# Kernel optimization log

Measured on AMD Instinct MI355X. Metric: run time of the kernel, lower is better.

Reference implementation:

```python
import jax, jax.numpy as jnp
import numpy as np

D_MODEL = 512
D_INNER = 1024  # expand * d_model
D_STATE = 128
D_CONV = 4
DT_RANK = 32
DT_MIN, DT_MAX, DT_FLOOR = 0.001, 0.1, 1e-4


def setup_inputs() -> dict:
    key = jax.random.key(0)
    ks = jax.random.split(key, 8)
    B, S = 2, 1024
    return {
        "x": jax.random.normal(ks[0], (B, S, D_MODEL), jnp.float32),
        "W_in": jax.random.normal(ks[1], (D_MODEL, 2 * D_INNER), jnp.float32) * 0.02,
        "conv_w": jax.random.normal(ks[2], (D_INNER, 1, D_CONV), jnp.float32) * 0.1,
        "conv_b": jnp.zeros((D_INNER,), jnp.float32),
        "W_x": jax.random.normal(ks[3], (D_INNER, DT_RANK + 2 * D_STATE), jnp.float32) * 0.02,
        "W_dt": jax.random.normal(ks[4], (DT_RANK, D_INNER), jnp.float32) * 0.02,
        "b_dt": jnp.zeros((D_INNER,), jnp.float32),
        "W_out": jax.random.normal(ks[5], (D_INNER, D_MODEL), jnp.float32) * 0.02,
    }


def _mamba_forward(x, W_in, conv_w, conv_b, W_x, W_dt, b_dt, W_out):
    Bsz, S, _ = x.shape
    xr = x @ W_in                              # [B,S,2*d_inner]
    xs, res = jnp.split(xr, 2, axis=-1)        # each [B,S,d_inner]

    # depthwise causal conv (torch pads both sides by d_conv-1 then truncates
    # to seq_len, which equals a left-pad-only causal conv)
    xc = xs.transpose(0, 2, 1)                 # [B,d_inner,S]
    xc = jax.lax.conv_general_dilated(
        xc, conv_w, window_strides=(1,), padding=[(D_CONV - 1, 0)],
        feature_group_count=D_INNER)
    u = (xc + conv_b[None, :, None]).transpose(0, 2, 1)  # [B,S,d_inner]

    dbl = u @ W_x                              # [B,S,dt_rank+2*d_state]
    dt, Bm, Cm = jnp.split(dbl, [DT_RANK, DT_RANK + D_STATE], axis=-1)
    dt = dt @ W_dt + b_dt                      # [B,S,d_inner]
    dt = jnp.clip(jax.nn.softplus(dt + DT_FLOOR), DT_MIN, DT_MAX)

    # selective scan: h_t = h_{t-1}*(1-dt_t) + x_t (outer) B_t ; y_t = h_t . C_t
    def step(h, inp):
        x_t, dt_t, B_t, C_t = inp              # [B,d_inner],[B,d_inner],[B,N],[B,N]
        h = h * (1.0 - dt_t)[..., None] + x_t[..., None] * B_t[:, None, :]
        y = jnp.einsum('bdn,bn->bd', h, C_t)
        return h, y

    h0 = jnp.zeros((Bsz, D_INNER, D_STATE), u.dtype)
    xs_t = (u.transpose(1, 0, 2), dt.transpose(1, 0, 2),
            Bm.transpose(1, 0, 2), Cm.transpose(1, 0, 2))
    _, ys = jax.lax.scan(step, h0, xs_t)       # ys: [S,B,d_inner]

    y = ys.transpose(1, 0, 2) + res
    return y @ W_out                           # [B,S,d_model]


def reference(x, W_in, conv_w, conv_b, W_x, W_dt, b_dt, W_out):
    return _mamba_forward(x, W_in, conv_w, conv_b, W_x, W_dt, b_dt, W_out)
```

## Files before the change

### kernel.cpp

```cpp
#include <hip/hip_runtime.h>
#include <math.h>

#define S_LEN 1024
#define BATCH 2
#define DM 512
#define DI 1024
#define DS 128
#define DTR 32
#define CL 64
#define NC (S_LEN / CL)

typedef unsigned short ushortT;
typedef __attribute__((ext_vector_type(8))) short short8;
typedef __attribute__((ext_vector_type(4))) float f32x4;

__device__ __forceinline__ ushortT f2b(float f) {
  unsigned u = __builtin_bit_cast(unsigned, f);
  unsigned r = (u + 0x7fff + ((u >> 16) & 1)) >> 16;
  return (ushortT)r;
}
__device__ __forceinline__ float b2f(ushortT h) {
  return __builtin_bit_cast(float, (unsigned)h << 16);
}

#define GLOAD16(g, l)                                                     \
  __builtin_amdgcn_global_load_lds(                                       \
      (const __attribute__((address_space(1))) void*)(g),                 \
      (__attribute__((address_space(3))) void*)(l), 16, 0, 0)

template<int MODE>
__global__ __launch_bounds__(256) void gemm64(
    const ushortT* __restrict__ A, const ushortT* __restrict__ Bt,
    void* __restrict__ Cout, int N, int K, int ldc, int nbx) {
  __shared__ ushortT As[2][64 * 32];
  __shared__ ushortT Bs[2][64 * 32];
  const int nwg = gridDim.x;
  const int bid = blockIdx.x;
  const int flat = (bid & 7) * (nwg >> 3) + (bid >> 3);
  const int bxi = flat % nbx, byi = flat / nbx;
  const int bm = byi * 64, bn = bxi * 64;
  const int tid = threadIdx.x;
  const int l = tid & 63, w = tid >> 6;
  const int wr = w >> 1, wc = w & 1;
  const int srow = tid >> 2, scol = (tid & 3) * 8;
  const ushortT* gA = A + (size_t)(bm + srow) * K + scol;
  const ushortT* gB = Bt + (size_t)(bn + srow) * K + scol;
  f32x4 acc[2][2] = {};
  const int nt = K >> 5;
  GLOAD16(gA, &As[0][(size_t)tid * 8]);
  GLOAD16(gB, &Bs[0][(size_t)tid * 8]);
  __syncthreads();
  int cur = 0;
  for (int t = 0; t < nt; ++t) {
    if (t + 1 < nt) {
      GLOAD16(gA + (t + 1) * 32, &As[cur ^ 1][(size_t)tid * 8]);
      GLOAD16(gB + (t + 1) * 32, &Bs[cur ^ 1][(size_t)tid * 8]);
    }
    short8 a[2], b[2];
#pragma unroll
    for (int m = 0; m < 2; ++m)
      a[m] = *(const short8*)&As[cur][(wr * 32 + m * 16 + (l & 15)) * 32 + (l >> 4) * 8];
#pragma unroll
    for (int n = 0; n < 2; ++n)
      b[n] = *(const short8*)&Bs[cur][(wc * 32 + n * 16 + (l & 15)) * 32 + (l >> 4) * 8];
#pragma unroll
    for (int m = 0; m < 2; ++m)
#pragma unroll
      for (int n = 0; n < 2; ++n)
        acc[m][n] = __builtin_amdgcn_mfma_f32_16x16x32_bf16(a[m], b[n], acc[m][n], 0, 0, 0);
    __syncthreads();
    cur ^= 1;
  }
#pragma unroll
  for (int m = 0; m < 2; ++m) {
    int grow = bm + wr * 32 + m * 16 + (l >> 4) * 4;
#pragma unroll
    for (int n = 0; n < 2; ++n) {
      int gcol = bn + wc * 32 + n * 16 + (l & 15);
      if (gcol >= N) continue;
#pragma unroll
      for (int i = 0; i < 4; ++i) {
        float v = acc[m][n][i];
        if (MODE == 1)
          ((ushortT*)Cout)[(size_t)(grow + i) * ldc + gcol] = f2b(v);
        else
          ((float*)Cout)[(size_t)(grow + i) * ldc + gcol] = v;
      }
    }
  }
}

__global__ __launch_bounds__(256) void prep_all(
    const float* __restrict__ W_in, const float* __restrict__ W_x,
    const float* __restrict__ W_out, const float* __restrict__ x,
    ushortT* __restrict__ Wt_in, ushortT* __restrict__ Wt_x,
    ushortT* __restrict__ Wt_out, ushortT* __restrict__ x_bf) {
  __shared__ float tb[32][33];
  int bid = blockIdx.x;
  int tx = threadIdx.x, ty = threadIdx.y;
  const float* in; ushortT* out; int K, N, bx, by;
  if (bid < 1024)      { in = W_in;  out = Wt_in;  K = 512;  N = 2048; bx = bid & 63; by = bid >> 6; }
  else if (bid < 1408) { int t2 = bid - 1024; in = W_x;   out = Wt_x;   K = 1024; N = 288;  bx = t2 % 12; by = t2 / 12; }
  else if (bid < 1920) { int t2 = bid - 1408; in = W_out; out = Wt_out; K = 1024; N = 512;  bx = t2 % 16; by = t2 / 16; }
  else {
    int i = (bid - 1920) * 256 + ty * 32 + tx;
    float4 v = ((const float4*)x)[i];
    ushort4 o; o.x = f2b(v.x); o.y = f2b(v.y); o.z = f2b(v.z); o.w = f2b(v.w);
    ((ushort4*)x_bf)[i] = o;
    return;
  }
  int n0 = bx * 32, k0 = by * 32;
  int flat = ty * 32 + tx;
  if (n0 < N) {
#pragma unroll
    for (int i = 0; i < 4; ++i)
      tb[ty + 8 * i][tx] = in[(size_t)(k0 + ty + 8 * i) * N + n0 + tx];
    __syncthreads();
#pragma unroll
    for (int j = 0; j < 2; ++j) {
      int idx = j * 256 + flat;
      int r = idx >> 4, c2 = idx & 15;
      ushort2 o;
      o.x = f2b(tb[2 * c2][r]);
      o.y = f2b(tb[2 * c2 + 1][r]);
      *(ushort2*)&out[(size_t)(n0 + r) * K + k0 + 2 * c2] = o;
    }
  } else {
    ushort2 z; z.x = 0; z.y = 0;
#pragma unroll
    for (int j = 0; j < 2; ++j) {
      int idx = j * 256 + flat;
      int r = idx >> 4, c2 = idx & 15;
      *(ushort2*)&out[(size_t)(n0 + r) * K + k0 + 2 * c2] = z;
    }
  }
}

__global__ __launch_bounds__(256) void conv_kernel(
    const ushortT* __restrict__ xr, const float* __restrict__ w,
    const float* __restrict__ b, ushortT* __restrict__ u) {
  int idx = blockIdx.x * blockDim.x + threadIdx.x;
  int g = idx & 255;
  int s = (idx >> 8) & (S_LEN - 1);
  int bb = idx >> 18;
  int d = g * 4;
  float4 bias = *(const float4*)&b[d];
  float4 w0 = *(const float4*)&w[(d + 0) * 4];
  float4 w1 = *(const float4*)&w[(d + 1) * 4];
  float4 w2 = *(const float4*)&w[(d + 2) * 4];
  float4 w3 = *(const float4*)&w[(d + 3) * 4];
  float a0 = bias.x, a1 = bias.y, a2 = bias.z, a3 = bias.w;
  const ushortT* xs = xr + (size_t)(bb * S_LEN) * (2 * DI) + d;
#pragma unroll
  for (int k = 0; k < 4; ++k) {
    int si = s - 3 + k;
    if (si >= 0) {
      ushort4 v = *(const ushort4*)&xs[(size_t)si * (2 * DI)];
      float wk0 = ((const float*)&w0)[k], wk1 = ((const float*)&w1)[k];
      float wk2 = ((const float*)&w2)[k], wk3 = ((const float*)&w3)[k];
      a0 = fmaf(b2f(v.x), wk0, a0);
      a1 = fmaf(b2f(v.y), wk1, a1);
      a2 = fmaf(b2f(v.z), wk2, a2);
      a3 = fmaf(b2f(v.w), wk3, a3);
    }
  }
  ushort4 o; o.x = f2b(a0); o.y = f2b(a1); o.z = f2b(a2); o.w = f2b(a3);
  *(ushort4*)&u[(size_t)idx * 4] = o;
}

__global__ __launch_bounds__(256) void megachunk(
    const float* __restrict__ dbl, const float* __restrict__ W_dt,
    const float* __restrict__ b_dt, const ushortT* __restrict__ u_bf,
    float* __restrict__ D, ushortT* __restrict__ ut,
    ushortT* __restrict__ zb) {
  __shared__ ushortT Btl[128][72];
  __shared__ float   Dl[64][66];
  __shared__ ushortT utl[64][72];
  __shared__ float   dtl[64][36];
  __shared__ ushortT Wl[32][68];
  const int t = threadIdx.x;
  const int dg = blockIdx.x, bc = blockIdx.y;
  const int b = bc >> 4, c = bc & 15;
  const size_t rowbase = (size_t)(b * S_LEN + c * CL) * DI + dg * 64;

#pragma unroll
  for (int j = 0; j < 8; ++j) {
    int idx4 = j * 256 + t;
    int s = idx4 >> 5, n4 = (idx4 & 31) * 4;
    float4 v = *(const float4*)&dbl[(size_t)(bc * 64 + s) * 288 + 32 + n4];
    Btl[n4][s] = f2b(v.x); Btl[n4 + 1][s] = f2b(v.y);
    Btl[n4 + 2][s] = f2b(v.z); Btl[n4 + 3][s] = f2b(v.w);
  }
#pragma unroll
  for (int j = 0; j < 2; ++j) {
    int idx4 = j * 256 + t;
    int s = idx4 >> 3, k4 = (idx4 & 7) * 4;
    *(float4*)&dtl[s][k4] = *(const float4*)&dbl[(size_t)(bc * 64 + s) * 288 + k4];
  }
#pragma unroll
  for (int j = 0; j < 4; ++j) {
    int idx2 = j * 256 + t;
    int k = idx2 >> 5, d2 = (idx2 & 31) * 2;
    float2 v = *(const float2*)&W_dt[(size_t)k * DI + dg * 64 + d2];
    Wl[k][d2] = f2b(v.x); Wl[k][d2 + 1] = f2b(v.y);
  }
  __syncthreads();

  {
    int d = t & 63, sq = t >> 6;
    float wreg[32];
#pragma unroll
    for (int k = 0; k < 32; ++k) wreg[k] = b2f(Wl[k][d]);
    float bias = b_dt[dg * 64 + d] + 1e-4f;
#pragma unroll 4
    for (int j = 0; j < 16; ++j) {
      int s = sq * 16 + j;
      float acc = bias;
#pragma unroll
      for (int k = 0; k < 32; ++k) acc = fmaf(dtl[s][k], wreg[k], acc);
      acc = (acc > 20.f) ? acc : log1pf(expf(acc));
      acc = fminf(fmaxf(acc, 0.001f), 0.1f);
      Dl[d][s] = 1.f - acc;
    }
  }
  __syncthreads();

  if (t < 64) {
    float cum = 1.f;
#pragma unroll 16
    for (int s = 0; s < CL; ++s) { cum *= Dl[t][s]; Dl[t][s] = cum; }
  }
  __syncthreads();

#pragma unroll
  for (int j = 0; j < 2; ++j) {
    int idx8 = j * 256 + t;
    int s = idx8 >> 3, d8 = (idx8 & 7) * 8;
    float4 raw = *(const float4*)&u_bf[rowbase + (size_t)s * DI + d8];
    const ushortT* up = (const ushortT*)&raw;
#pragma unroll
    for (int k = 0; k < 8; ++k)
      utl[d8 + k][s] = f2b(b2f(up[k]) / Dl[d8 + k][s]);
  }
  __syncthreads();

  {
    const int l = t & 63, w = t >> 6;
    f32x4 acc[8] = {};
#pragma unroll
    for (int kk = 0; kk < 2; ++kk) {
      short8 a = *(const short8*)&utl[w * 16 + (l & 15)][kk * 32 + (l >> 4) * 8];
#pragma unroll
      for (int n = 0; n < 8; ++n) {
        short8 bb = *(const short8*)&Btl[n * 16 + (l & 15)][kk * 32 + (l >> 4) * 8];
        acc[n] = __builtin_amdgcn_mfma_f32_16x16x32_bf16(a, bb, acc[n], 0, 0, 0);
      }
    }
#pragma unroll
    for (int n = 0; n < 8; ++n) {
      int gn = n * 16 + (l & 15);
#pragma unroll
      for (int i = 0; i < 4; ++i) {
        int d = dg * 64 + w * 16 + (l >> 4) * 4 + i;
        zb[(((size_t)(b * DI + d)) * NC + c) * 128 + gn] = f2b(acc[n][i]);
      }
    }
  }

#pragma unroll
  for (int j = 0; j < 4; ++j) {
    int idx4 = j * 256 + t;
    int s = idx4 >> 4, d4 = (idx4 & 15) * 4;
    float4 v;
    v.x = Dl[d4][s]; v.y = Dl[d4 + 1][s]; v.z = Dl[d4 + 2][s]; v.w = Dl[d4 + 3][s];
    *(float4*)&D[rowbase + (size_t)s * DI + d4] = v;
  }
#pragma unroll
  for (int j = 0; j < 2; ++j) {
    int idx8 = j * 256 + t;
    int d = idx8 >> 3, s8 = (idx8 & 7) * 8;
    float4 v; ushortT* vp = (ushortT*)&v;
#pragma unroll
    for (int k = 0; k < 8; ++k) vp[k] = utl[d][s8 + k];
    *(float4*)&ut[((size_t)bc * DI + dg * 64 + d) * CL + s8] = v;
  }
}

__global__ __launch_bounds__(256) void scan_pass2(
    const ushortT* __restrict__ zb, const float* __restrict__ D,
    ushortT* __restrict__ hstb) {
  int wid = (blockIdx.x * blockDim.x + threadIdx.x) >> 6;
  int lane = threadIdx.x & 63;
  int b = wid >> 10, d = wid & (DI - 1);
  size_t base = (size_t)wid * NC * 128;
  float h0 = 0.f, h1 = 0.f;
#pragma unroll
  for (int c = 0; c < NC; ++c) {
    float dend = D[((size_t)(b * S_LEN + c * CL + CL - 1)) * DI + d];
    ushort2 z2 = *(const ushort2*)&zb[base + c * 128 + 2 * lane];
    ushort2 he;
    he.x = f2b(h0); he.y = f2b(h1);
    *(ushort2*)&hstb[base + c * 128 + 2 * lane] = he;
    h0 = dend * (h0 + b2f(z2.x));
    h1 = dend * (h1 + b2f(z2.y));
  }
}

__global__ __launch_bounds__(256) void gemm_y(
    const float* __restrict__ dbl, const ushortT* __restrict__ ut,
    const ushortT* __restrict__ hstb, const float* __restrict__ D,
    const ushortT* __restrict__ xr_bf, ushortT* __restrict__ yr) {
  __shared__ ushortT Bl[64][136];
  __shared__ ushortT Cl[64][136];
  __shared__ ushortT Gl[64][72];
  const int tid = threadIdx.x;
  const int l = tid & 63, w = tid >> 6;
  const int bc = blockIdx.y, d0 = blockIdx.x * 64;
  const int b = bc >> 4, c = bc & 15;
  const int brow = b * S_LEN + c * CL;
  short8 ub[2][4];
#pragma unroll
  for (int kk = 0; kk < 2; ++kk)
#pragma unroll
    for (int n = 0; n < 4; ++n) {
      int d = d0 + n * 16 + (l & 15);
      ub[kk][n] = *(const short8*)&ut[((size_t)bc * DI + d) * CL + kk * 32 + (l >> 4) * 8];
    }
#pragma unroll
  for (int j = 0; j < 16; ++j) {
    int idx4 = j * 256 + tid;
    int row = idx4 >> 6, c4 = (idx4 & 63) * 4;
    float4 v = *(const float4*)&dbl[(size_t)(bc * 64 + row) * 288 + 32 + c4];
    ushortT o0 = f2b(v.x), o1 = f2b(v.y), o2 = f2b(v.z), o3 = f2b(v.w);
    if (c4 < 128) { Bl[row][c4] = o0; Bl[row][c4+1] = o1; Bl[row][c4+2] = o2; Bl[row][c4+3] = o3; }
    else { int cc = c4 - 128; Cl[row][cc] = o0; Cl[row][cc+1] = o1; Cl[row][cc+2] = o2; Cl[row][cc+3] = o3; }
  }
  __syncthreads();
  {
    f32x4 gacc[4] = {};
#pragma unroll
    for (int kk = 0; kk < 4; ++kk) {
      short8 a = *(const short8*)&Cl[w * 16 + (l & 15)][kk * 32 + (l >> 4) * 8];
#pragma unroll
      for (int nf = 0; nf < 4; ++nf) {
        short8 bb = *(const short8*)&Bl[nf * 16 + (l & 15)][kk * 32 + (l >> 4) * 8];
        gacc[nf] = __builtin_amdgcn_mfma_f32_16x16x32_bf16(a, bb, gacc[nf], 0, 0, 0);
      }
    }
#pragma unroll
    for (int nf = 0; nf < 4; ++nf) {
      int s = nf * 16 + (l & 15);
#pragma unroll
      for (int i = 0; i < 4; ++i) {
        int tr = w * 16 + (l >> 4) * 4 + i;
        Gl[tr][s] = f2b((s <= tr) ? gacc[nf][i] : 0.f);
      }
    }
  }
  __syncthreads();
  f32x4 acc[4] = {};
#pragma unroll
  for (int kk = 0; kk < 2; ++kk) {
    short8 a = *(const short8*)&Gl[w * 16 + (l & 15)][kk * 32 + (l >> 4) * 8];
#pragma unroll
    for (int n = 0; n < 4; ++n)
      acc[n] = __builtin_amdgcn_mfma_f32_16x16x32_bf16(a, ub[kk][n], acc[n], 0, 0, 0);
  }
#pragma unroll
  for (int kk = 0; kk < 4; ++kk) {
    short8 a = *(const short8*)&Cl[w * 16 + (l & 15)][kk * 32 + (l >> 4) * 8];
#pragma unroll
    for (int n = 0; n < 4; ++n) {
      int d = d0 + n * 16 + (l & 15);
      short8 bb = *(const short8*)&hstb[((size_t)(b * DI + d)) * (NC * 128) + c * 128 + kk * 32 + (l >> 4) * 8];
      acc[n] = __builtin_amdgcn_mfma_f32_16x16x32_bf16(a, bb, acc[n], 0, 0, 0);
    }
  }
#pragma unroll
  for (int n = 0; n < 4; ++n) {
    int d = d0 + n * 16 + (l & 15);
#pragma unroll
    for (int i = 0; i < 4; ++i) {
      int gr = brow + w * 16 + (l >> 4) * 4 + i;
      float Dv = D[(size_t)gr * DI + d];
      float res = b2f(xr_bf[(size_t)gr * 2048 + 1024 + d]);
      yr[(size_t)gr * DI + d] = f2b(acc[n][i] * Dv + res);
    }
  }
}

extern "C" void kernel_launch(void* const* d_in, const int* in_sizes, int n_in,
                              void* d_out, int out_size, void* d_ws, size_t ws_size,
                              hipStream_t stream) {
  const float* x      = (const float*)d_in[0];
  const float* W_in   = (const float*)d_in[1];
  const float* conv_w = (const float*)d_in[2];
  const float* conv_b = (const float*)d_in[3];
  const float* W_x    = (const float*)d_in[4];
  const float* W_dt   = (const float*)d_in[5];
  const float* b_dt   = (const float*)d_in[6];
  const float* W_out  = (const float*)d_in[7];
  float* out = (float*)d_out;
  float* ws = (float*)d_ws;

  ushortT* xr_bf = (ushortT*)ws;
  ushortT* u_bf  = (ushortT*)(ws + 2097152);
  float*   dbl   = ws + 3145728;
  float*   Dc    = ws + 3735552;
  ushortT* ut    = (ushortT*)(ws + 5832704);
  ushortT* zb    = (ushortT*)(ws + 6881280);
  ushortT* hstb  = (ushortT*)(ws + 8978432);
  ushortT* x_bf  = (ushortT*)(ws + 11075584);
  ushortT* Wt_in = (ushortT*)(ws + 11599872);
  ushortT* Wt_x  = (ushortT*)(ws + 12124160);
  ushortT* Wt_out= (ushortT*)(ws + 12320768);
  ushortT* yr_bf = (ushortT*)(ws + 12582912);

  dim3 blk(256);
  prep_all<<<2944, dim3(32, 8), 0, stream>>>(W_in, W_x, W_out, x,
                                             Wt_in, Wt_x, Wt_out, x_bf);
  gemm64<1><<<1024, blk, 0, stream>>>(x_bf, Wt_in, xr_bf, 2 * DI, DM, 2 * DI, 32);
  conv_kernel<<<2048, blk, 0, stream>>>(xr_bf, conv_w, conv_b, u_bf);
  gemm64<0><<<160, blk, 0, stream>>>(u_bf, Wt_x, dbl, DTR + 2 * DS, DI, DTR + 2 * DS, 5);
  megachunk<<<dim3(16, 32), blk, 0, stream>>>(dbl, W_dt, b_dt, u_bf, Dc, ut, zb);
  scan_pass2<<<512, blk, 0, stream>>>(zb, Dc, hstb);
  gemm_y<<<dim3(16, 32), blk, 0, stream>>>(dbl, ut, hstb, Dc, xr_bf, yr_bf);
  gemm64<0><<<256, blk, 0, stream>>>(yr_bf, Wt_out, out, DM, DI, DM, 8);
}
```

Measured before the change: 96.92 us.

## Store decay in bf16, reorder chunk-state layout, stage gemm_y operands in LDS

The cumulative decay array D is now written and read as bf16 instead of fp32, which halves its traffic across megachunk, scan_pass2 and gemm_y. The zb/hstb chunk-state tensors are relaid out as [b][chunk][d][n], so each gemm_y block reads one contiguous tile. gemm_y now loads ut, hstb and D tiles into shared memory with coalesced 16-byte loads instead of strided per-lane global reads. The costs are lower precision in the decay factors and more LDS use per block, which may reduce occupancy.

```diff
diff --git a/kernel.cpp b/kernel.cpp
--- a/kernel.cpp
+++ b/kernel.cpp
@@ -171,7 +171,7 @@
 __global__ __launch_bounds__(256) void megachunk(
     const float* __restrict__ dbl, const float* __restrict__ W_dt,
     const float* __restrict__ b_dt, const ushortT* __restrict__ u_bf,
-    float* __restrict__ D, ushortT* __restrict__ ut,
+    ushortT* __restrict__ D, ushortT* __restrict__ ut,
     ushortT* __restrict__ zb) {
   __shared__ ushortT Btl[128][72];
   __shared__ float   Dl[64][66];
@@ -262,18 +262,19 @@
 #pragma unroll
       for (int i = 0; i < 4; ++i) {
         int d = dg * 64 + w * 16 + (l >> 4) * 4 + i;
-        zb[(((size_t)(b * DI + d)) * NC + c) * 128 + gn] = f2b(acc[n][i]);
+        zb[(((size_t)(b * NC + c)) * DI + d) * 128 + gn] = f2b(acc[n][i]);
       }
     }
   }
 
 #pragma unroll
-  for (int j = 0; j < 4; ++j) {
-    int idx4 = j * 256 + t;
-    int s = idx4 >> 4, d4 = (idx4 & 15) * 4;
-    float4 v;
-    v.x = Dl[d4][s]; v.y = Dl[d4 + 1][s]; v.z = Dl[d4 + 2][s]; v.w = Dl[d4 + 3][s];
-    *(float4*)&D[rowbase + (size_t)s * DI + d4] = v;
+  for (int j = 0; j < 2; ++j) {
+    int idx8 = j * 256 + t;
+    int s = idx8 >> 3, d8 = (idx8 & 7) * 8;
+    float4 v; ushortT* vp = (ushortT*)&v;
+#pragma unroll
+    for (int k = 0; k < 8; ++k) vp[k] = f2b(Dl[d8 + k][s]);
+    *(float4*)&D[rowbase + (size_t)s * DI + d8] = v;
   }
 #pragma unroll
   for (int j = 0; j < 2; ++j) {
@@ -287,20 +288,20 @@
 }
 
 __global__ __launch_bounds__(256) void scan_pass2(
-    const ushortT* __restrict__ zb, const float* __restrict__ D,
+    const ushortT* __restrict__ zb, const ushortT* __restrict__ D,
     ushortT* __restrict__ hstb) {
   int wid = (blockIdx.x * blockDim.x + threadIdx.x) >> 6;
   int lane = threadIdx.x & 63;
   int b = wid >> 10, d = wid & (DI - 1);
-  size_t base = (size_t)wid * NC * 128;
   float h0 = 0.f, h1 = 0.f;
 #pragma unroll
   for (int c = 0; c < NC; ++c) {
-    float dend = D[((size_t)(b * S_LEN + c * CL + CL - 1)) * DI + d];
-    ushort2 z2 = *(const ushort2*)&zb[base + c * 128 + 2 * lane];
+    float dend = b2f(D[((size_t)(b * S_LEN + c * CL + CL - 1)) * DI + d]);
+    size_t addr = (((size_t)(b * NC + c)) * DI + d) * 128 + 2 * lane;
+    ushort2 z2 = *(const ushort2*)&zb[addr];
     ushort2 he;
     he.x = f2b(h0); he.y = f2b(h1);
-    *(ushort2*)&hstb[base + c * 128 + 2 * lane] = he;
+    *(ushort2*)&hstb[addr] = he;
     h0 = dend * (h0 + b2f(z2.x));
     h1 = dend * (h1 + b2f(z2.y));
   }
@@ -308,24 +309,40 @@
 
 __global__ __launch_bounds__(256) void gemm_y(
     const float* __restrict__ dbl, const ushortT* __restrict__ ut,
-    const ushortT* __restrict__ hstb, const float* __restrict__ D,
+    const ushortT* __restrict__ hstb, const ushortT* __restrict__ D,
     const ushortT* __restrict__ xr_bf, ushortT* __restrict__ yr) {
   __shared__ ushortT Bl[64][136];
   __shared__ ushortT Cl[64][136];
   __shared__ ushortT Gl[64][72];
+  __shared__ ushortT Ul[64][72];
+  __shared__ ushortT Hl[64][136];
+  __shared__ ushortT Dl2[64][72];
   const int tid = threadIdx.x;
   const int l = tid & 63, w = tid >> 6;
   const int bc = blockIdx.y, d0 = blockIdx.x * 64;
   const int b = bc >> 4, c = bc & 15;
   const int brow = b * S_LEN + c * CL;
-  short8 ub[2][4];
-#pragma unroll
-  for (int kk = 0; kk < 2; ++kk)
-#pragma unroll
-    for (int n = 0; n < 4; ++n) {
-      int d = d0 + n * 16 + (l & 15);
-      ub[kk][n] = *(const short8*)&ut[((size_t)bc * DI + d) * CL + kk * 32 + (l >> 4) * 8];
-    }
+#pragma unroll
+  for (int j = 0; j < 2; ++j) {
+    int idx4 = j * 256 + tid;
+    int dr = idx4 >> 3, s8 = (idx4 & 7) * 8;
+    float4 v = *(const float4*)&ut[((size_t)bc * DI + d0 + dr) * CL + s8];
+    *(float4*)&Ul[dr][s8] = v;
+  }
+#pragma unroll
+  for (int j = 0; j < 4; ++j) {
+    int idx4 = j * 256 + tid;
+    int dr = idx4 >> 4, n8 = (idx4 & 15) * 8;
+    float4 v = *(const float4*)&hstb[(((size_t)(b * NC + c)) * DI + d0 + dr) * 128 + n8];
+    *(float4*)&Hl[dr][n8] = v;
+  }
+#pragma unroll
+  for (int j = 0; j < 2; ++j) {
+    int idx4 = j * 256 + tid;
+    int tr = idx4 >> 3, d8 = (idx4 & 7) * 8;
+    float4 v = *(const float4*)&D[((size_t)(brow + tr)) * DI + d0 + d8];
+    *(float4*)&Dl2[tr][d8] = v;
+  }
 #pragma unroll
   for (int j = 0; j < 16; ++j) {
     int idx4 = j * 256 + tid;
@@ -363,26 +380,29 @@
   for (int kk = 0; kk < 2; ++kk) {
     short8 a = *(const short8*)&Gl[w * 16 + (l & 15)][kk * 32 + (l >> 4) * 8];
 #pragma unroll
-    for (int n = 0; n < 4; ++n)
-      acc[n] = __builtin_amdgcn_mfma_f32_16x16x32_bf16(a, ub[kk][n], acc[n], 0, 0, 0);
+    for (int n = 0; n < 4; ++n) {
+      short8 bb = *(const short8*)&Ul[n * 16 + (l & 15)][kk * 32 + (l >> 4) * 8];
+      acc[n] = __builtin_amdgcn_mfma_f32_16x16x32_bf16(a, bb, acc[n], 0, 0, 0);
+    }
   }
 #pragma unroll
   for (int kk = 0; kk < 4; ++kk) {
     short8 a = *(const short8*)&Cl[w * 16 + (l & 15)][kk * 32 + (l >> 4) * 8];
 #pragma unroll
     for (int n = 0; n < 4; ++n) {
-      int d = d0 + n * 16 + (l & 15);
-      short8 bb = *(const short8*)&hstb[((size_t)(b * DI + d)) * (NC * 128) + c * 128 + kk * 32 + (l >> 4) * 8];
+      short8 bb = *(const short8*)&Hl[n * 16 + (l & 15)][kk * 32 + (l >> 4) * 8];
       acc[n] = __builtin_amdgcn_mfma_f32_16x16x32_bf16(a, bb, acc[n], 0, 0, 0);
     }
   }
 #pragma unroll
   for (int n = 0; n < 4; ++n) {
-    int d = d0 + n * 16 + (l & 15);
+    int dl = n * 16 + (l & 15);
+    int d = d0 + dl;
 #pragma unroll
     for (int i = 0; i < 4; ++i) {
-      int gr = brow + w * 16 + (l >> 4) * 4 + i;
-      float Dv = D[(size_t)gr * DI + d];
+      int tl = w * 16 + (l >> 4) * 4 + i;
+      int gr = brow + tl;
+      float Dv = b2f(Dl2[tl][dl]);
       float res = b2f(xr_bf[(size_t)gr * 2048 + 1024 + d]);
       yr[(size_t)gr * DI + d] = f2b(acc[n][i] * Dv + res);
     }
@@ -406,7 +426,7 @@
   ushortT* xr_bf = (ushortT*)ws;
   ushortT* u_bf  = (ushortT*)(ws + 2097152);
   float*   dbl   = ws + 3145728;
-  float*   Dc    = ws + 3735552;
+  ushortT* Dc    = (ushortT*)(ws + 3735552);
   ushortT* ut    = (ushortT*)(ws + 5832704);
   ushortT* zb    = (ushortT*)(ws + 6881280);
   ushortT* hstb  = (ushortT*)(ws + 8978432);
```

Measured after the change: 94.13 us. -2.9%, faster.
